# Kernel tuning notes

Measured on AMD Instinct MI355X. Metric: run time of the kernel, lower is better.

## Reference

```python
import jax, jax.numpy as jnp
import numpy as np
from jax import lax

AGG_HOPS = 3
RANK_K = 10
NEG = -1e9


def _aggregate(embs, agg_w, agg_b, W_last, b_last):
    # GIKT-style multi-hop mean aggregation: embs[j] has shape [B, n1..nj, D]
    embs = list(embs)
    for i in range(AGG_HOPS):
        for j in range(AGG_HOPS - i):
            s = jnp.mean(embs[j + 1], axis=-2) + embs[j]
            embs[j] = jnp.tanh(s @ agg_w[j].T + agg_b[j])
    return jnp.tanh(embs[0] @ W_last.T + b_last)


def _hops(nodes0, tabA, tabB):
    # alternating bipartite neighbor expansion: [B] -> [B,n] -> [B,n,n] -> ...
    lst = [nodes0]
    for i in range(AGG_HOPS):
        tab = tabA if i % 2 == 0 else tabB
        lst.append(tab[lst[-1]])
    return lst


def _forward(user, question, response, mask, q_neighbors, s_neighbors, u_neighbors,
             q_neighbors_2, qs_index, emb_question, emb_question_2, emb_skill,
             emb_user, emb_response, w1_q, w2_q, W_ih, W_hh, b_ih, b_hh,
             agg_w, agg_b, W_agg_last, b_agg_last, W_query, b_query, W_key, b_key,
             W_w, b_w, W_fusion, b_fusion):
    B, T = question.shape
    D = emb_question.shape[1]
    emb_q_all = emb_question[question]  # [B,T,D], used for recap similarity
    wA, wB = W_w[0, :D], W_w[0, D:]     # MLP_W(cat(Q,K)) = Q@wA + K@wB + b

    def predict(qs_concat, states, svalid):
        ql = (qs_concat @ W_query.T + b_query) @ wA          # [B,Lq]
        kl = (states @ W_key.T + b_key) @ wB                 # [B,Ls]
        logit = ql[:, :, None] + kl[:, None, :] + b_w[0]     # [B,Lq,Ls]
        logit = jnp.where(svalid[:, None, :], logit, NEG)
        Lq, Ls = logit.shape[1], logit.shape[2]
        alpha = jax.nn.softmax(logit.reshape(B, -1), axis=1).reshape(B, Lq, Ls)
        g = jnp.einsum('bqd,bsd->bqs', qs_concat, states)
        return jax.nn.sigmoid(jnp.sum(alpha * g, axis=(1, 2)))

    def step(carry, t):
        h, c, sh = carry
        q_t, u_t, r_t = question[:, t], user[:, t], response[:, t]
        m = (mask[:, t] == 1)[:, None]  # [B,1]
        # question-skill GNN branch
        embs_q = [(emb_question if i % 2 == 0 else emb_skill)[n]
                  for i, n in enumerate(_hops(q_t, q_neighbors, s_neighbors))]
        e1 = jnp.where(m, _aggregate(embs_q, agg_w, agg_b, W_agg_last, b_agg_last),
                       emb_question[q_t])
        # user-question GNN branch
        embs_u = [(emb_user if i % 2 == 0 else emb_question_2)[n]
                  for i, n in enumerate(_hops(u_t, u_neighbors, q_neighbors_2))]
        e2 = jnp.where(m, _aggregate(embs_u, agg_w, agg_b, W_agg_last, b_agg_last),
                       emb_question_2[q_t])
        e_hat = w1_q * e1 + w2_q * e2
        e_t = jax.nn.relu(jnp.concatenate([e_hat, emb_response[r_t]], axis=1)
                          @ W_fusion.T + b_fusion)
        # masked LSTMCell (torch gate order i,f,g,o); dropout in eval mode
        gates = e_t @ W_ih.T + b_ih + h @ W_hh.T + b_hh
        gi, gf, gg, go = jnp.split(gates, 4, axis=1)
        c2 = jax.nn.sigmoid(gf) * c + jax.nn.sigmoid(gi) * jnp.tanh(gg)
        h2 = jax.nn.sigmoid(go) * jnp.tanh(c2)
        h = jnp.where(m, h2, h)
        c = jnp.where(m, c2, c)
        sh = lax.dynamic_update_slice(sh, h[:, None, :], (0, t, 0))
        # next question + its related skills
        q_next = question[:, t + 1]
        emb_qn = emb_question[q_next]
        qs_concat = jnp.concatenate([emb_qn[:, None, :], emb_skill[qs_index[q_next]]], axis=1)
        # soft recap: top-k past states by (detached) question similarity
        scores = lax.stop_gradient(jnp.einsum('btd,bd->bt', emb_q_all, emb_qn))
        valid_t = jnp.arange(T) < t
        scores = jnp.where(valid_t[None, :], scores, NEG)
        _, idx = lax.top_k(scores, RANK_K)                    # [B,K]
        sel = jnp.take_along_axis(sh, idx[:, :, None], axis=1)  # [B,K,D]
        svalid = jnp.concatenate([jnp.ones((B, 1), bool), valid_t[idx]], axis=1)
        states = jnp.concatenate([h[:, None, :], sel], axis=1)  # [B,1+K,D]
        y = predict(qs_concat, states, svalid)
        return (h, c, sh), y

    h0 = jnp.zeros((B, D), jnp.float32)
    sh0 = jnp.zeros((B, T, D), jnp.float32)
    _, ys = lax.scan(step, (h0, h0, sh0), jnp.arange(T - 1))
    return jnp.concatenate([jnp.full((B, 1), 0.5, jnp.float32), ys.T], axis=1)


def setup_inputs() -> dict:
    B, T, D = 32, 50, 100
    NQ, NS, NU = 20000, 500, 10000
    NBR, SPQ = 6, 4
    key = jax.random.key(0)
    ks = iter(jax.random.split(key, 48))
    nrm = lambda shape, sc: jax.random.normal(next(ks), shape, jnp.float32) * sc
    ri = lambda shape, hi: jax.random.randint(next(ks), shape, 0, hi, jnp.int32)
    s = 1.0 / float(np.sqrt(D))
    return {
        'user': ri((B, T), NU), 'question': ri((B, T), NQ),
        'response': ri((B, T), 2), 'mask': ri((B, T), 2),
        'q_neighbors': ri((NQ, NBR), NS), 's_neighbors': ri((NS, NBR), NQ),
        'u_neighbors': ri((NU, NBR), NQ), 'q_neighbors_2': ri((NQ, NBR), NU),
        'qs_index': ri((NQ, SPQ), NS),
        'emb_question': nrm((NQ, D), 0.1), 'emb_question_2': nrm((NQ, D), 0.1),
        'emb_skill': nrm((NS, D), 0.1), 'emb_user': nrm((NU, D), 0.1),
        'emb_response': nrm((2, D), 0.1),
        'w1_q': jnp.float32(0.5), 'w2_q': jnp.float32(0.5),
        'W_ih': nrm((4 * D, D), s), 'W_hh': nrm((4 * D, D), s),
        'b_ih': jnp.zeros((4 * D,), jnp.float32), 'b_hh': jnp.zeros((4 * D,), jnp.float32),
        'agg_w': nrm((3, D, D), s), 'agg_b': jnp.zeros((3, D), jnp.float32),
        'W_agg_last': nrm((D, D), s), 'b_agg_last': jnp.zeros((D,), jnp.float32),
        'W_query': nrm((D, D), s), 'b_query': jnp.zeros((D,), jnp.float32),
        'W_key': nrm((D, D), s), 'b_key': jnp.zeros((D,), jnp.float32),
        'W_w': nrm((1, 2 * D), s), 'b_w': jnp.zeros((1,), jnp.float32),
        'W_fusion': nrm((D, 2 * D), s), 'b_fusion': jnp.zeros((D,), jnp.float32),
    }


def reference(user, question, response, mask, q_neighbors, s_neighbors, u_neighbors,
              q_neighbors_2, qs_index, emb_question, emb_question_2, emb_skill,
              emb_user, emb_response, w1_q, w2_q, W_ih, W_hh, b_ih, b_hh,
              agg_w, agg_b, W_agg_last, b_agg_last, W_query, b_query, W_key, b_key,
              W_w, b_w, W_fusion, b_fusion):
    return _forward(user, question, response, mask, q_neighbors, s_neighbors,
                    u_neighbors, q_neighbors_2, qs_index, emb_question,
                    emb_question_2, emb_skill, emb_user, emb_response, w1_q, w2_q,
                    W_ih, W_hh, b_ih, b_hh, agg_w, agg_b, W_agg_last, b_agg_last,
                    W_query, b_query, W_key, b_key, W_w, b_w, W_fusion, b_fusion)
```

## Files before the change

### kernel.cpp

```cpp
#include <hip/hip_runtime.h>
#include <hip/hip_bf16.h>

#define BSZ 32
#define TT 50
#define TS 49

#define OFF_VQ    0u
#define OFF_VK    128u
#define OFF_SC    256u
#define OFF_BIHH  288u
#define OFF_GPRE  704u
#define OFF_QL    627904u
#define OFF_IDX   640448u
#define OFF_NV    656128u
#define OFF_QSC   657696u
#define OFF_E1    1441696u
#define OFF_E2    1598496u

#define RLF(v,l) __uint_as_float(__builtin_amdgcn_readlane(__float_as_uint(v), (l)))

__device__ __forceinline__ float tanh_fast(float x) {
    float e = __expf(2.f * x);
    return 1.f - __fdividef(2.f, e + 1.f);
}
__device__ __forceinline__ float sigm_fast(float x) {
    return __fdividef(1.f, 1.f + __expf(-x));
}
__device__ __forceinline__ float dot4(float4 a, float4 b) {
    return a.x*b.x + a.y*b.y + a.z*b.z + a.w*b.w;
}
__device__ __forceinline__ float dot100(const float* __restrict__ w, const float* __restrict__ x) {
    float acc = 0.f;
    for (int k = 0; k < 100; k += 4)
        acc += dot4(*(const float4*)(w + k), *(const float4*)(x + k));
    return acc;
}

__global__ __launch_bounds__(256) void kprep(
    const float* __restrict__ wq, const float* __restrict__ bq,
    const float* __restrict__ wk, const float* __restrict__ bk,
    const float* __restrict__ ww, const float* __restrict__ bw,
    const float* __restrict__ w1, const float* __restrict__ w2,
    const float* __restrict__ bih, const float* __restrict__ bhh,
    float* __restrict__ WS)
{
    int tid = threadIdx.x;
    for (int i = tid; i < 400; i += 256) WS[OFF_BIHH + i] = bih[i] + bhh[i];
    if (tid < 100) {
        float a1 = 0.f, a2 = 0.f;
        for (int d = 0; d < 100; ++d) {
            a1 += ww[d]       * wq[d*100 + tid];
            a2 += ww[100 + d] * wk[d*100 + tid];
        }
        WS[OFF_VQ + tid] = a1;
        WS[OFF_VK + tid] = a2;
    }
    if (tid == 0) {
        float cq = 0.f, ck = 0.f;
        for (int d = 0; d < 100; ++d) {
            cq += bq[d] * ww[d];
            ck += bk[d] * ww[100 + d];
        }
        WS[OFF_SC + 0] = cq;
        WS[OFF_SC + 1] = ck;
        WS[OFF_SC + 2] = bw[0];
        WS[OFF_SC + 3] = w1[0];
        WS[OFF_SC + 4] = w2[0];
    }
}

__global__ __launch_bounds__(256) void kagg(
    const int* __restrict__ user, const int* __restrict__ question, const int* __restrict__ mask,
    const int* __restrict__ qnbr, const int* __restrict__ snbr,
    const int* __restrict__ unbr, const int* __restrict__ qnbr2,
    const float* __restrict__ embQ, const float* __restrict__ embQ2, const float* __restrict__ embS,
    const float* __restrict__ embU,
    const float* __restrict__ aggw, const float* __restrict__ aggb,
    const float* __restrict__ wlast, const float* __restrict__ blast,
    float* __restrict__ WS)
{
    int bid = blockIdx.x;
    int pair = bid >> 1, which = bid & 1;
    int b = pair / TS, t = pair - b*TS;
    int tid = threadIdx.x;
    int mm = mask[b*TT + t];
    float* outE = WS + (which ? OFF_E2 : OFF_E1) + (size_t)pair*100;

    if (mm != 1) {
        int q_t = question[b*TT + t];
        const float* src = which ? embQ2 : embQ;
        if (tid < 100) outE[tid] = src[(size_t)q_t*100 + tid];
        return;
    }

    int root = which ? user[b*TT + t] : question[b*TT + t];
    const int*   tabA = which ? unbr  : qnbr;
    const int*   tabB = which ? qnbr2 : snbr;
    const float* embE = which ? embU  : embQ;
    const float* embO = which ? embQ2 : embS;

    __shared__ __align__(16) float b2in[36*108];
    __shared__ __align__(16) float x1[6*108];
    __shared__ float s2[600], v1a[600], v1b[600];
    __shared__ __align__(16) float x0[104], v0a[104], v0b[104];
    __shared__ int n1[8], n2[36], n3[216];

    if (tid < 6) n1[tid] = tabA[root*6 + tid];
    __syncthreads();
    if (tid < 36) n2[tid] = tabB[n1[tid/6]*6 + (tid % 6)];
    __syncthreads();
    if (tid < 216) n3[tid] = tabA[n2[tid/6]*6 + (tid % 6)];
    __syncthreads();
    for (int e = tid; e < 3600; e += 256) {
        int v = e / 100, d = e - v*100;
        float acc = embE[(size_t)n2[v]*100 + d];
        float s3 = 0.f;
        const int* p = n3 + v*6;
        for (int c = 0; c < 6; ++c) s3 += embO[(size_t)p[c]*100 + d];
        b2in[v*108 + d] = acc + s3 * (1.f/6.f);
    }
    for (int e = tid; e < 600; e += 256) {
        int a = e / 100, d = e - a*100;
        float acc = embO[(size_t)n1[a]*100 + d];
        float s = 0.f;
        for (int c = 0; c < 6; ++c) s += embE[(size_t)n2[a*6 + c]*100 + d];
        x1[a*108 + d] = acc + s * (1.f/6.f);
    }
    if (tid < 100) {
        float acc = embE[(size_t)root*100 + tid];
        float s = 0.f;
        for (int a = 0; a < 6; ++a) s += embO[(size_t)n1[a]*100 + tid];
        x0[tid] = acc + s * (1.f/6.f);
    }
    __syncthreads();
    if (tid < 150) {
        int dblk = tid / 6, a = tid % 6, d0 = dblk*4;
        const float* wp = aggw + 20000 + d0*100;
        const float* xb = b2in + a*648;
        float acc[4][6];
        #pragma unroll
        for (int r = 0; r < 4; ++r)
            #pragma unroll
            for (int c = 0; c < 6; ++c) acc[r][c] = 0.f;
        #pragma unroll
        for (int j = 0; j < 25; ++j) {
            float4 r0 = *(const float4*)(wp + 4*j);
            float4 r1 = *(const float4*)(wp + 100 + 4*j);
            float4 r2 = *(const float4*)(wp + 200 + 4*j);
            float4 r3 = *(const float4*)(wp + 300 + 4*j);
            #pragma unroll
            for (int c = 0; c < 6; ++c) {
                float4 x = *(const float4*)(xb + c*108 + 4*j);
                acc[0][c] += dot4(r0, x);
                acc[1][c] += dot4(r1, x);
                acc[2][c] += dot4(r2, x);
                acc[3][c] += dot4(r3, x);
            }
        }
        #pragma unroll
        for (int r = 0; r < 4; ++r) {
            float bia = aggb[200 + d0 + r];
            float o = 0.f;
            #pragma unroll
            for (int c = 0; c < 6; ++c) o += tanh_fast(bia + acc[r][c]);
            s2[a*100 + d0 + r] = o;
        }
    } else if (tid < 200) {
        int d0 = (tid - 150)*2;
        const float* wp = aggw + 10000 + d0*100;
        float acc[2][6];
        #pragma unroll
        for (int r = 0; r < 2; ++r)
            #pragma unroll
            for (int c = 0; c < 6; ++c) acc[r][c] = 0.f;
        #pragma unroll
        for (int j = 0; j < 25; ++j) {
            float4 r0 = *(const float4*)(wp + 4*j);
            float4 r1 = *(const float4*)(wp + 100 + 4*j);
            #pragma unroll
            for (int c = 0; c < 6; ++c) {
                float4 x = *(const float4*)(x1 + c*108 + 4*j);
                acc[0][c] += dot4(r0, x);
                acc[1][c] += dot4(r1, x);
            }
        }
        #pragma unroll
        for (int r = 0; r < 2; ++r)
            #pragma unroll
            for (int c = 0; c < 6; ++c)
                v1a[c*100 + d0 + r] = tanh_fast(aggb[100 + d0 + r] + acc[r][c]);
    } else if (tid < 250) {
        int d0 = (tid - 200)*2;
        const float* wp = aggw + d0*100;
        float a0 = 0.f, a1 = 0.f;
        #pragma unroll
        for (int j = 0; j < 25; ++j) {
            float4 x  = *(const float4*)(x0 + 4*j);
            a0 += dot4(*(const float4*)(wp + 4*j), x);
            a1 += dot4(*(const float4*)(wp + 100 + 4*j), x);
        }
        v0a[d0]   = tanh_fast(aggb[d0] + a0);
        v0a[d0+1] = tanh_fast(aggb[d0+1] + a1);
    }
    __syncthreads();
    for (int e = tid; e < 600; e += 256) {
        int a = e / 100, d = e - a*100;
        x1[a*108 + d] = v1a[a*100 + d] + s2[a*100 + d]*(1.f/6.f);
    }
    if (tid < 100) {
        float s = 0.f;
        for (int a = 0; a < 6; ++a) s += v1a[a*100 + tid];
        x0[tid] = v0a[tid] + s*(1.f/6.f);
    }
    __syncthreads();
    if (tid < 50) {
        int d0 = tid*2;
        const float* wp = aggw + 10000 + d0*100;
        float acc[2][6];
        #pragma unroll
        for (int r = 0; r < 2; ++r)
            #pragma unroll
            for (int c = 0; c < 6; ++c) acc[r][c] = 0.f;
        #pragma unroll
        for (int j = 0; j < 25; ++j) {
            float4 r0 = *(const float4*)(wp + 4*j);
            float4 r1 = *(const float4*)(wp + 100 + 4*j);
            #pragma unroll
            for (int c = 0; c < 6; ++c) {
                float4 x = *(const float4*)(x1 + c*108 + 4*j);
                acc[0][c] += dot4(r0, x);
                acc[1][c] += dot4(r1, x);
            }
        }
        #pragma unroll
        for (int r = 0; r < 2; ++r)
            #pragma unroll
            for (int c = 0; c < 6; ++c)
                v1b[c*100 + d0 + r] = tanh_fast(aggb[100 + d0 + r] + acc[r][c]);
    } else if (tid >= 64 && tid < 114) {
        int d0 = (tid - 64)*2;
        const float* wp = aggw + d0*100;
        float a0 = 0.f, a1 = 0.f;
        #pragma unroll
        for (int j = 0; j < 25; ++j) {
            float4 x  = *(const float4*)(x0 + 4*j);
            a0 += dot4(*(const float4*)(wp + 4*j), x);
            a1 += dot4(*(const float4*)(wp + 100 + 4*j), x);
        }
        v0b[d0]   = tanh_fast(aggb[d0] + a0);
        v0b[d0+1] = tanh_fast(aggb[d0+1] + a1);
    }
    __syncthreads();
    if (tid < 100) {
        float s = 0.f;
        for (int a = 0; a < 6; ++a) s += v1b[a*100 + tid];
        x0[tid] = v0b[tid] + s*(1.f/6.f);
    }
    __syncthreads();
    if (tid < 50) {
        int d0 = tid*2;
        const float* wp = aggw + d0*100;
        float a0 = 0.f, a1 = 0.f;
        #pragma unroll
        for (int j = 0; j < 25; ++j) {
            float4 x  = *(const float4*)(x0 + 4*j);
            a0 += dot4(*(const float4*)(wp + 4*j), x);
            a1 += dot4(*(const float4*)(wp + 100 + 4*j), x);
        }
        v0a[d0]   = tanh_fast(aggb[d0] + a0);
        v0a[d0+1] = tanh_fast(aggb[d0+1] + a1);
    }
    __syncthreads();
    if (tid < 50) {
        int d0 = tid*2;
        const float* wp = wlast + d0*100;
        float a0 = 0.f, a1 = 0.f;
        #pragma unroll
        for (int j = 0; j < 25; ++j) {
            float4 x  = *(const float4*)(v0a + 4*j);
            a0 += dot4(*(const float4*)(wp + 4*j), x);
            a1 += dot4(*(const float4*)(wp + 100 + 4*j), x);
        }
        outE[d0]   = tanh_fast(blast[d0] + a0);
        outE[d0+1] = tanh_fast(blast[d0+1] + a1);
    }
}

__global__ __launch_bounds__(256) void kfuse(
    const int* __restrict__ question, const int* __restrict__ response,
    const int* __restrict__ qsidx,
    const float* __restrict__ embQ, const float* __restrict__ embS, const float* __restrict__ embR,
    const float* __restrict__ wfus, const float* __restrict__ bfus,
    const float* __restrict__ wih,
    float* __restrict__ WS)
{
    int bid = blockIdx.x;
    int b = bid / TS, t = bid - b*TS;
    int tid = threadIdx.x;
    size_t bt = (size_t)b*TS + t;

    __shared__ __align__(16) float sEIN[200], sET[104], sEQN[104];
    __shared__ float sQSCm[500], sScore[52];

    int r_t = response[b*TT + t];
    int qn  = question[b*TT + t + 1];
    float w1 = WS[OFF_SC + 3], w2s = WS[OFF_SC + 4];
    if (tid < 100)
        sEIN[tid] = w1*WS[OFF_E1 + bt*100 + tid] + w2s*WS[OFF_E2 + bt*100 + tid];
    else if (tid < 200)
        sEIN[tid] = embR[r_t*100 + (tid - 100)];
    __syncthreads();
    if (tid < 100) {
        float acc = bfus[tid];
        const float* wr = wfus + tid*200;
        for (int k = 0; k < 200; k += 4)
            acc += dot4(*(const float4*)(wr + k), *(const float4*)(sEIN + k));
        sET[tid] = fmaxf(acc, 0.f);
    } else if (tid >= 128 && tid < 228) {
        sEQN[tid - 128] = embQ[(size_t)qn*100 + (tid - 128)];
    }
    __syncthreads();
    for (int o = tid; o < 400; o += 256)
        WS[OFF_GPRE + bt*400 + o] = WS[OFF_BIHH + o] + dot100(wih + o*100, sET);
    for (int i = tid; i < 500; i += 256) {
        int q = i / 100, d = i - q*100;
        float val = (q == 0) ? sEQN[d] : embS[(size_t)qsidx[qn*4 + (q-1)]*100 + d];
        sQSCm[i] = val;
        WS[OFF_QSC + bt*500 + i] = val;
    }
    if (tid >= 200 && tid < 200 + TT) {
        int tp = tid - 200;
        if (tp < t) {
            int qq = question[b*TT + tp];
            float acc = 0.f;
            for (int k = 0; k < 100; ++k) acc += embQ[(size_t)qq*100 + k] * sEQN[k];
            sScore[tp] = acc;
        }
    }
    __syncthreads();
    if (tid < 5) {
        float acc = WS[OFF_SC + 0];
        for (int k = 0; k < 100; ++k) acc += sQSCm[tid*100 + k] * WS[OFF_VQ + k];
        WS[OFF_QL + bt*8 + tid] = acc;
    }
    if (tid == 64) {
        int nv = t < 10 ? t : 10;
        ((int*)(WS + OFF_NV))[bt] = nv;
        int* idxp = (int*)(WS + OFF_IDX) + bt*10;
        unsigned long long taken = 0ull;
        for (int p = 0; p < 10; ++p) {
            int bi = 0;
            if (p < nv) {
                float best = -3.0e38f;
                for (int tp2 = 0; tp2 < t; ++tp2) {
                    if (!((taken >> tp2) & 1ull) && sScore[tp2] > best) { best = sScore[tp2]; bi = tp2; }
                }
                taken |= (1ull << bi);
            }
            idxp[p] = bi;
        }
    }
}

__global__ __launch_bounds__(512) void kseq(
    const int* __restrict__ mask, const float* __restrict__ whh,
    const float* __restrict__ WS, float* __restrict__ out)
{
    int b = blockIdx.x, tid = threadIdx.x, lane = tid & 63;
    __shared__ float sQSCall[TS*500];
    __shared__ float sSH[TS*100];
    __shared__ float sQLall[TS*8];
    __shared__ int   sIdxAll[TS*10];
    __shared__ int   sNvAll[TS];
    __shared__ int   sMask[TT];
    __shared__ float sH[104], sC[104], sG[400], sVKl[104];
    __shared__ float sKL[12], sGv[64];

    const float* gGPRE = WS + OFF_GPRE;
    size_t b0 = (size_t)b*TS;

    float4 wv[25];
    if (tid < 400) {
        #pragma unroll
        for (int j = 0; j < 25; ++j) wv[j] = *(const float4*)(whh + tid*100 + 4*j);
    }
    float gpre = (tid < 400) ? gGPRE[b0*400 + tid] : 0.f;

    for (int i = tid; i < TS*500; i += 512) sQSCall[i] = WS[OFF_QSC + b0*500 + i];
    for (int i = tid; i < TS*8;   i += 512) sQLall[i]  = WS[OFF_QL + b0*8 + i];
    for (int i = tid; i < TS*10;  i += 512) sIdxAll[i] = ((const int*)(WS + OFF_IDX))[b0*10 + i];
    for (int i = tid; i < TS;     i += 512) sNvAll[i]  = ((const int*)(WS + OFF_NV))[b0 + i];
    if (tid < TT) sMask[tid] = mask[b*TT + tid];
    for (int i = tid; i < 104; i += 512) { sH[i] = 0.f; sC[i] = 0.f; sVKl[i] = (i < 100) ? WS[OFF_VK + i] : 0.f; }
    float ck = WS[OFF_SC + 1], bw = WS[OFF_SC + 2];
    if (tid == 0) out[b*TT] = 0.5f;
    __syncthreads();

    for (int t = 0; t < TS; ++t) {
        float gpre_nx = 0.f;
        if (tid < 400 && t + 1 < TS) gpre_nx = gGPRE[(b0 + t + 1)*400 + tid];

        float hA = sH[lane];
        float hB = sH[64 + (lane % 36)];
        if (tid < 400) {
            float a0 = 0.f, a1 = 0.f, a2 = 0.f, a3 = 0.f;
            #pragma unroll
            for (int j = 0; j < 25; ++j) {
                const int kb = 4*j;
                float h0, h1, h2, h3;
                if (kb < 64) {
                    h0 = RLF(hA, kb);   h1 = RLF(hA, kb+1);
                    h2 = RLF(hA, kb+2); h3 = RLF(hA, kb+3);
                } else {
                    h0 = RLF(hB, kb-64); h1 = RLF(hB, kb-63);
                    h2 = RLF(hB, kb-62); h3 = RLF(hB, kb-61);
                }
                a0 = fmaf(h0, wv[j].x, a0);
                a1 = fmaf(h1, wv[j].y, a1);
                a2 = fmaf(h2, wv[j].z, a2);
                a3 = fmaf(h3, wv[j].w, a3);
            }
            sG[tid] = (a0 + a1) + (a2 + a3) + gpre;
        }
        __syncthreads();
        if (tid < 100) {
            int mm = sMask[t];
            float gi = sG[tid], gf = sG[100+tid], gg = sG[200+tid], go = sG[300+tid];
            float c2 = sigm_fast(gf)*sC[tid] + sigm_fast(gi)*tanh_fast(gg);
            float h2 = sigm_fast(go)*tanh_fast(c2);
            if (mm == 1) { sH[tid] = h2; sC[tid] = c2; }
            sSH[t*100 + tid] = sH[tid];
        }
        __syncthreads();
        int nv = sNvAll[t];
        int k0 = tid & 15, slot = tid >> 4;
        const float* xq = sQSCall + t*500;
        #pragma unroll
        for (int p = 0; p < 3; ++p) {
            int id = p*32 + slot;
            float acc = 0.f;
            bool on = false, isKL = false; int q = 0, s = 0;
            if (id < 66) {
                isKL = id < 11;
                if (isKL) s = id; else { q = (id - 11) / 11; s = (id - 11) % 11; }
                if (s <= nv) {
                    on = true;
                    const float* st = (s == 0) ? sH : (sSH + sIdxAll[t*10 + s - 1]*100);
                    const float* xp = isKL ? sVKl : (xq + q*100);
                    #pragma unroll
                    for (int jj = 0; jj < 7; ++jj) {
                        int k = k0 + 16*jj;
                        if (k < 100) acc = fmaf(st[k], xp[k], acc);
                    }
                }
            }
            acc += __shfl_xor(acc, 1); acc += __shfl_xor(acc, 2);
            acc += __shfl_xor(acc, 4); acc += __shfl_xor(acc, 8);
            if (on && k0 == 0) { if (isKL) sKL[s] = acc + ck; else sGv[q*11 + s] = acc; }
        }
        __syncthreads();
        if (tid < 64) {
            int nst = nv + 1;
            int q = tid / 11, s = tid - q*11;
            bool valid = (tid < 55) && (s < nst);
            float lg = valid ? (sQLall[t*8 + q] + sKL[s] + bw) : -3.0e38f;
            float mx = lg;
            #pragma unroll
            for (int m = 1; m < 64; m <<= 1) mx = fmaxf(mx, __shfl_xor(mx, m));
            float e  = valid ? __expf(lg - mx) : 0.f;
            float gv = valid ? sGv[q*11 + s] : 0.f;
            float se = e, sg = e*gv;
            #pragma unroll
            for (int m = 1; m < 64; m <<= 1) { se += __shfl_xor(se, m); sg += __shfl_xor(sg, m); }
            if (tid == 0) out[b*TT + t + 1] = __fdividef(1.f, 1.f + __expf(-__fdividef(sg, se)));
        }
        gpre = gpre_nx;
        __syncthreads();
    }
}

extern "C" void kernel_launch(void* const* d_in, const int* in_sizes, int n_in,
                              void* d_out, int out_size, void* d_ws, size_t ws_size,
                              hipStream_t stream) {
    const int* user      = (const int*)d_in[0];
    const int* question  = (const int*)d_in[1];
    const int* response  = (const int*)d_in[2];
    const int* mask      = (const int*)d_in[3];
    const int* qnbr      = (const int*)d_in[4];
    const int* snbr      = (const int*)d_in[5];
    const int* unbr      = (const int*)d_in[6];
    const int* qnbr2     = (const int*)d_in[7];
    const int* qsidx     = (const int*)d_in[8];
    const float* embQ    = (const float*)d_in[9];
    const float* embQ2   = (const float*)d_in[10];
    const float* embS    = (const float*)d_in[11];
    const float* embU    = (const float*)d_in[12];
    const float* embR    = (const float*)d_in[13];
    const float* w1      = (const float*)d_in[14];
    const float* w2      = (const float*)d_in[15];
    const float* wih     = (const float*)d_in[16];
    const float* whh     = (const float*)d_in[17];
    const float* bih     = (const float*)d_in[18];
    const float* bhh     = (const float*)d_in[19];
    const float* aggw    = (const float*)d_in[20];
    const float* aggb    = (const float*)d_in[21];
    const float* wlast   = (const float*)d_in[22];
    const float* blast   = (const float*)d_in[23];
    const float* wq      = (const float*)d_in[24];
    const float* bq      = (const float*)d_in[25];
    const float* wk      = (const float*)d_in[26];
    const float* bk      = (const float*)d_in[27];
    const float* ww      = (const float*)d_in[28];
    const float* bwp     = (const float*)d_in[29];
    const float* wfus    = (const float*)d_in[30];
    const float* bfus    = (const float*)d_in[31];
    float* WS = (float*)d_ws;
    float* out = (float*)d_out;

    hipLaunchKernelGGL(kprep, dim3(1), dim3(256), 0, stream,
                       wq, bq, wk, bk, ww, bwp, w1, w2, bih, bhh, WS);
    hipLaunchKernelGGL(kagg, dim3(2*BSZ*TS), dim3(256), 0, stream,
                       user, question, mask, qnbr, snbr, unbr, qnbr2,
                       embQ, embQ2, embS, embU, aggw, aggb, wlast, blast, WS);
    hipLaunchKernelGGL(kfuse, dim3(BSZ*TS), dim3(256), 0, stream,
                       question, response, qsidx, embQ, embS, embR,
                       wfus, bfus, wih, WS);
    hipLaunchKernelGGL(kseq, dim3(BSZ), dim3(512), 0, stream,
                       mask, whh, WS, out);
}
```

Before: 489.2 us.

## Drop prep kernel, widen aggregation blocks, overlap attention with LSTM steps

Measured after the change: 438.4 us. 10.4% less time.

```diff
diff --git a/kernel.cpp b/kernel.cpp
--- a/kernel.cpp
+++ b/kernel.cpp
@@ -4,18 +4,15 @@
 #define BSZ 32
 #define TT 50
 #define TS 49
-
-#define OFF_VQ    0u
-#define OFF_VK    128u
-#define OFF_SC    256u
-#define OFF_BIHH  288u
-#define OFF_GPRE  704u
-#define OFF_QL    627904u
-#define OFF_IDX   640448u
-#define OFF_NV    656128u
-#define OFF_QSC   657696u
-#define OFF_E1    1441696u
-#define OFF_E2    1598496u
+#define PH 101
+
+#define OFF_GPRE  0u
+#define OFF_QL    627200u
+#define OFF_IDX   639744u
+#define OFF_NV    655424u
+#define OFF_QSC   656992u
+#define OFF_E1    1440992u
+#define OFF_E2    1597792u
 
 #define RLF(v,l) __uint_as_float(__builtin_amdgcn_readlane(__float_as_uint(v), (l)))
 
@@ -36,40 +33,7 @@
     return acc;
 }
 
-__global__ __launch_bounds__(256) void kprep(
-    const float* __restrict__ wq, const float* __restrict__ bq,
-    const float* __restrict__ wk, const float* __restrict__ bk,
-    const float* __restrict__ ww, const float* __restrict__ bw,
-    const float* __restrict__ w1, const float* __restrict__ w2,
-    const float* __restrict__ bih, const float* __restrict__ bhh,
-    float* __restrict__ WS)
-{
-    int tid = threadIdx.x;
-    for (int i = tid; i < 400; i += 256) WS[OFF_BIHH + i] = bih[i] + bhh[i];
-    if (tid < 100) {
-        float a1 = 0.f, a2 = 0.f;
-        for (int d = 0; d < 100; ++d) {
-            a1 += ww[d]       * wq[d*100 + tid];
-            a2 += ww[100 + d] * wk[d*100 + tid];
-        }
-        WS[OFF_VQ + tid] = a1;
-        WS[OFF_VK + tid] = a2;
-    }
-    if (tid == 0) {
-        float cq = 0.f, ck = 0.f;
-        for (int d = 0; d < 100; ++d) {
-            cq += bq[d] * ww[d];
-            ck += bk[d] * ww[100 + d];
-        }
-        WS[OFF_SC + 0] = cq;
-        WS[OFF_SC + 1] = ck;
-        WS[OFF_SC + 2] = bw[0];
-        WS[OFF_SC + 3] = w1[0];
-        WS[OFF_SC + 4] = w2[0];
-    }
-}
-
-__global__ __launch_bounds__(256) void kagg(
+__global__ __launch_bounds__(384, 5) void kagg(
     const int* __restrict__ user, const int* __restrict__ question, const int* __restrict__ mask,
     const int* __restrict__ qnbr, const int* __restrict__ snbr,
     const int* __restrict__ unbr, const int* __restrict__ qnbr2,
@@ -101,7 +65,8 @@
 
     __shared__ __align__(16) float b2in[36*108];
     __shared__ __align__(16) float x1[6*108];
-    __shared__ float s2[600], v1a[600], v1b[600];
+    __shared__ float s2v1b[600];
+    __shared__ float v1a[600];
     __shared__ __align__(16) float x0[104], v0a[104], v0b[104];
     __shared__ int n1[8], n2[36], n3[216];
 
@@ -111,7 +76,7 @@
     __syncthreads();
     if (tid < 216) n3[tid] = tabA[n2[tid/6]*6 + (tid % 6)];
     __syncthreads();
-    for (int e = tid; e < 3600; e += 256) {
+    for (int e = tid; e < 3600; e += 384) {
         int v = e / 100, d = e - v*100;
         float acc = embE[(size_t)n2[v]*100 + d];
         float s3 = 0.f;
@@ -119,7 +84,7 @@
         for (int c = 0; c < 6; ++c) s3 += embO[(size_t)p[c]*100 + d];
         b2in[v*108 + d] = acc + s3 * (1.f/6.f);
     }
-    for (int e = tid; e < 600; e += 256) {
+    for (int e = tid; e < 600; e += 384) {
         int a = e / 100, d = e - a*100;
         float acc = embO[(size_t)n1[a]*100 + d];
         float s = 0.f;
@@ -133,46 +98,35 @@
         x0[tid] = acc + s * (1.f/6.f);
     }
     __syncthreads();
-    if (tid < 150) {
-        int dblk = tid / 6, a = tid % 6, d0 = dblk*4;
+    if (tid < 300) {
+        int dblk = tid / 6, a = tid - dblk*6, d0 = dblk*2;
         const float* wp = aggw + 20000 + d0*100;
         const float* xb = b2in + a*648;
-        float acc[4][6];
-        #pragma unroll
-        for (int r = 0; r < 4; ++r)
-            #pragma unroll
-            for (int c = 0; c < 6; ++c) acc[r][c] = 0.f;
+        float a0[6], a1[6];
+        #pragma unroll
+        for (int c = 0; c < 6; ++c) { a0[c] = 0.f; a1[c] = 0.f; }
         #pragma unroll
         for (int j = 0; j < 25; ++j) {
             float4 r0 = *(const float4*)(wp + 4*j);
             float4 r1 = *(const float4*)(wp + 100 + 4*j);
-            float4 r2 = *(const float4*)(wp + 200 + 4*j);
-            float4 r3 = *(const float4*)(wp + 300 + 4*j);
             #pragma unroll
             for (int c = 0; c < 6; ++c) {
                 float4 x = *(const float4*)(xb + c*108 + 4*j);
-                acc[0][c] += dot4(r0, x);
-                acc[1][c] += dot4(r1, x);
-                acc[2][c] += dot4(r2, x);
-                acc[3][c] += dot4(r3, x);
-            }
-        }
-        #pragma unroll
-        for (int r = 0; r < 4; ++r) {
-            float bia = aggb[200 + d0 + r];
-            float o = 0.f;
-            #pragma unroll
-            for (int c = 0; c < 6; ++c) o += tanh_fast(bia + acc[r][c]);
-            s2[a*100 + d0 + r] = o;
-        }
-    } else if (tid < 200) {
-        int d0 = (tid - 150)*2;
+                a0[c] += dot4(r0, x);
+                a1[c] += dot4(r1, x);
+            }
+        }
+        float bi0 = aggb[200 + d0], bi1 = aggb[200 + d0 + 1];
+        float o0 = 0.f, o1 = 0.f;
+        #pragma unroll
+        for (int c = 0; c < 6; ++c) { o0 += tanh_fast(bi0 + a0[c]); o1 += tanh_fast(bi1 + a1[c]); }
+        s2v1b[a*100 + d0] = o0; s2v1b[a*100 + d0 + 1] = o1;
+    } else if (tid < 350) {
+        int d0 = (tid - 300)*2;
         const float* wp = aggw + 10000 + d0*100;
-        float acc[2][6];
-        #pragma unroll
-        for (int r = 0; r < 2; ++r)
-            #pragma unroll
-            for (int c = 0; c < 6; ++c) acc[r][c] = 0.f;
+        float a0[6], a1[6];
+        #pragma unroll
+        for (int c = 0; c < 6; ++c) { a0[c] = 0.f; a1[c] = 0.f; }
         #pragma unroll
         for (int j = 0; j < 25; ++j) {
             float4 r0 = *(const float4*)(wp + 4*j);
@@ -180,32 +134,36 @@
             #pragma unroll
             for (int c = 0; c < 6; ++c) {
                 float4 x = *(const float4*)(x1 + c*108 + 4*j);
-                acc[0][c] += dot4(r0, x);
-                acc[1][c] += dot4(r1, x);
-            }
-        }
-        #pragma unroll
-        for (int r = 0; r < 2; ++r)
-            #pragma unroll
-            for (int c = 0; c < 6; ++c)
-                v1a[c*100 + d0 + r] = tanh_fast(aggb[100 + d0 + r] + acc[r][c]);
-    } else if (tid < 250) {
-        int d0 = (tid - 200)*2;
+                a0[c] += dot4(r0, x);
+                a1[c] += dot4(r1, x);
+            }
+        }
+        #pragma unroll
+        for (int c = 0; c < 6; ++c) {
+            v1a[c*100 + d0]     = tanh_fast(aggb[100 + d0] + a0[c]);
+            v1a[c*100 + d0 + 1] = tanh_fast(aggb[100 + d0 + 1] + a1[c]);
+        }
+    } else if (tid < 375) {
+        int d0 = (tid - 350)*4;
         const float* wp = aggw + d0*100;
-        float a0 = 0.f, a1 = 0.f;
-        #pragma unroll
-        for (int j = 0; j < 25; ++j) {
-            float4 x  = *(const float4*)(x0 + 4*j);
+        float a0 = 0.f, a1 = 0.f, a2 = 0.f, a3 = 0.f;
+        #pragma unroll
+        for (int j = 0; j < 25; ++j) {
+            float4 x = *(const float4*)(x0 + 4*j);
             a0 += dot4(*(const float4*)(wp + 4*j), x);
             a1 += dot4(*(const float4*)(wp + 100 + 4*j), x);
+            a2 += dot4(*(const float4*)(wp + 200 + 4*j), x);
+            a3 += dot4(*(const float4*)(wp + 300 + 4*j), x);
         }
         v0a[d0]   = tanh_fast(aggb[d0] + a0);
         v0a[d0+1] = tanh_fast(aggb[d0+1] + a1);
-    }
-    __syncthreads();
-    for (int e = tid; e < 600; e += 256) {
+        v0a[d0+2] = tanh_fast(aggb[d0+2] + a2);
+        v0a[d0+3] = tanh_fast(aggb[d0+3] + a3);
+    }
+    __syncthreads();
+    for (int e = tid; e < 600; e += 384) {
         int a = e / 100, d = e - a*100;
-        x1[a*108 + d] = v1a[a*100 + d] + s2[a*100 + d]*(1.f/6.f);
+        x1[a*108 + d] = v1a[a*100 + d] + s2v1b[a*100 + d]*(1.f/6.f);
     }
     if (tid < 100) {
         float s = 0.f;
@@ -216,11 +174,9 @@
     if (tid < 50) {
         int d0 = tid*2;
         const float* wp = aggw + 10000 + d0*100;
-        float acc[2][6];
-        #pragma unroll
-        for (int r = 0; r < 2; ++r)
-            #pragma unroll
-            for (int c = 0; c < 6; ++c) acc[r][c] = 0.f;
+        float a0[6], a1[6];
+        #pragma unroll
+        for (int c = 0; c < 6; ++c) { a0[c] = 0.f; a1[c] = 0.f; }
         #pragma unroll
         for (int j = 0; j < 25; ++j) {
             float4 r0 = *(const float4*)(wp + 4*j);
@@ -228,61 +184,73 @@
             #pragma unroll
             for (int c = 0; c < 6; ++c) {
                 float4 x = *(const float4*)(x1 + c*108 + 4*j);
-                acc[0][c] += dot4(r0, x);
-                acc[1][c] += dot4(r1, x);
-            }
-        }
-        #pragma unroll
-        for (int r = 0; r < 2; ++r)
-            #pragma unroll
-            for (int c = 0; c < 6; ++c)
-                v1b[c*100 + d0 + r] = tanh_fast(aggb[100 + d0 + r] + acc[r][c]);
-    } else if (tid >= 64 && tid < 114) {
-        int d0 = (tid - 64)*2;
+                a0[c] += dot4(r0, x);
+                a1[c] += dot4(r1, x);
+            }
+        }
+        #pragma unroll
+        for (int c = 0; c < 6; ++c) {
+            s2v1b[c*100 + d0]     = tanh_fast(aggb[100 + d0] + a0[c]);
+            s2v1b[c*100 + d0 + 1] = tanh_fast(aggb[100 + d0 + 1] + a1[c]);
+        }
+    } else if (tid >= 64 && tid < 89) {
+        int d0 = (tid - 64)*4;
         const float* wp = aggw + d0*100;
-        float a0 = 0.f, a1 = 0.f;
-        #pragma unroll
-        for (int j = 0; j < 25; ++j) {
-            float4 x  = *(const float4*)(x0 + 4*j);
+        float a0 = 0.f, a1 = 0.f, a2 = 0.f, a3 = 0.f;
+        #pragma unroll
+        for (int j = 0; j < 25; ++j) {
+            float4 x = *(const float4*)(x0 + 4*j);
             a0 += dot4(*(const float4*)(wp + 4*j), x);
             a1 += dot4(*(const float4*)(wp + 100 + 4*j), x);
+            a2 += dot4(*(const float4*)(wp + 200 + 4*j), x);
+            a3 += dot4(*(const float4*)(wp + 300 + 4*j), x);
         }
         v0b[d0]   = tanh_fast(aggb[d0] + a0);
         v0b[d0+1] = tanh_fast(aggb[d0+1] + a1);
+        v0b[d0+2] = tanh_fast(aggb[d0+2] + a2);
+        v0b[d0+3] = tanh_fast(aggb[d0+3] + a3);
     }
     __syncthreads();
     if (tid < 100) {
         float s = 0.f;
-        for (int a = 0; a < 6; ++a) s += v1b[a*100 + tid];
+        for (int a = 0; a < 6; ++a) s += s2v1b[a*100 + tid];
         x0[tid] = v0b[tid] + s*(1.f/6.f);
     }
     __syncthreads();
-    if (tid < 50) {
-        int d0 = tid*2;
+    if (tid < 25) {
+        int d0 = tid*4;
         const float* wp = aggw + d0*100;
-        float a0 = 0.f, a1 = 0.f;
-        #pragma unroll
-        for (int j = 0; j < 25; ++j) {
-            float4 x  = *(const float4*)(x0 + 4*j);
+        float a0 = 0.f, a1 = 0.f, a2 = 0.f, a3 = 0.f;
+        #pragma unroll
+        for (int j = 0; j < 25; ++j) {
+            float4 x = *(const float4*)(x0 + 4*j);
             a0 += dot4(*(const float4*)(wp + 4*j), x);
             a1 += dot4(*(const float4*)(wp + 100 + 4*j), x);
+            a2 += dot4(*(const float4*)(wp + 200 + 4*j), x);
+            a3 += dot4(*(const float4*)(wp + 300 + 4*j), x);
         }
         v0a[d0]   = tanh_fast(aggb[d0] + a0);
         v0a[d0+1] = tanh_fast(aggb[d0+1] + a1);
-    }
-    __syncthreads();
-    if (tid < 50) {
-        int d0 = tid*2;
+        v0a[d0+2] = tanh_fast(aggb[d0+2] + a2);
+        v0a[d0+3] = tanh_fast(aggb[d0+3] + a3);
+    }
+    __syncthreads();
+    if (tid < 25) {
+        int d0 = tid*4;
         const float* wp = wlast + d0*100;
-        float a0 = 0.f, a1 = 0.f;
-        #pragma unroll
-        for (int j = 0; j < 25; ++j) {
-            float4 x  = *(const float4*)(v0a + 4*j);
+        float a0 = 0.f, a1 = 0.f, a2 = 0.f, a3 = 0.f;
+        #pragma unroll
+        for (int j = 0; j < 25; ++j) {
+            float4 x = *(const float4*)(v0a + 4*j);
             a0 += dot4(*(const float4*)(wp + 4*j), x);
             a1 += dot4(*(const float4*)(wp + 100 + 4*j), x);
+            a2 += dot4(*(const float4*)(wp + 200 + 4*j), x);
+            a3 += dot4(*(const float4*)(wp + 300 + 4*j), x);
         }
         outE[d0]   = tanh_fast(blast[d0] + a0);
         outE[d0+1] = tanh_fast(blast[d0+1] + a1);
+        outE[d0+2] = tanh_fast(blast[d0+2] + a2);
+        outE[d0+3] = tanh_fast(blast[d0+3] + a3);
     }
 }
 
@@ -290,8 +258,10 @@
     const int* __restrict__ question, const int* __restrict__ response,
     const int* __restrict__ qsidx,
     const float* __restrict__ embQ, const float* __restrict__ embS, const float* __restrict__ embR,
+    const float* __restrict__ w1p, const float* __restrict__ w2p,
     const float* __restrict__ wfus, const float* __restrict__ bfus,
-    const float* __restrict__ wih,
+    const float* __restrict__ wih, const float* __restrict__ bih, const float* __restrict__ bhh,
+    const float* __restrict__ wq, const float* __restrict__ bq, const float* __restrict__ ww,
     float* __restrict__ WS)
 {
     int bid = blockIdx.x;
@@ -299,16 +269,18 @@
     int tid = threadIdx.x;
     size_t bt = (size_t)b*TS + t;
 
-    __shared__ __align__(16) float sEIN[200], sET[104], sEQN[104];
-    __shared__ float sQSCm[500], sScore[52];
+    __shared__ __align__(16) float sEIN[200], sET[104], sEQN[104], sVQ[104];
+    __shared__ float sWW[200], sQSCm[500], sScore[56], sCq[1];
 
     int r_t = response[b*TT + t];
     int qn  = question[b*TT + t + 1];
-    float w1 = WS[OFF_SC + 3], w2s = WS[OFF_SC + 4];
+    float w1 = w1p[0], w2 = w2p[0];
     if (tid < 100)
-        sEIN[tid] = w1*WS[OFF_E1 + bt*100 + tid] + w2s*WS[OFF_E2 + bt*100 + tid];
+        sEIN[tid] = w1*WS[OFF_E1 + bt*100 + tid] + w2*WS[OFF_E2 + bt*100 + tid];
     else if (tid < 200)
         sEIN[tid] = embR[r_t*100 + (tid - 100)];
+    else
+        for (int i = tid - 200; i < 200; i += 56) sWW[i] = ww[i];
     __syncthreads();
     if (tid < 100) {
         float acc = bfus[tid];
@@ -316,34 +288,55 @@
         for (int k = 0; k < 200; k += 4)
             acc += dot4(*(const float4*)(wr + k), *(const float4*)(sEIN + k));
         sET[tid] = fmaxf(acc, 0.f);
-    } else if (tid >= 128 && tid < 228) {
-        sEQN[tid - 128] = embQ[(size_t)qn*100 + (tid - 128)];
-    }
-    __syncthreads();
-    for (int o = tid; o < 400; o += 256)
-        WS[OFF_GPRE + bt*400 + o] = WS[OFF_BIHH + o] + dot100(wih + o*100, sET);
-    for (int i = tid; i < 500; i += 256) {
-        int q = i / 100, d = i - q*100;
-        float val = (q == 0) ? sEQN[d] : embS[(size_t)qsidx[qn*4 + (q-1)]*100 + d];
-        sQSCm[i] = val;
-        WS[OFF_QSC + bt*500 + i] = val;
-    }
-    if (tid >= 200 && tid < 200 + TT) {
+    } else if (tid < 200) {
+        int k = tid - 100;
+        float acc = 0.f;
+        for (int d = 0; d < 100; ++d) acc += sWW[d]*wq[d*100 + k];
+        sVQ[k] = acc;
+    } else if (tid == 200) {
+        float acc = 0.f;
+        for (int d = 0; d < 100; ++d) acc += bq[d]*sWW[d];
+        sCq[0] = acc;
+    } else if (tid >= 201 && tid < 251) {
+        int d = tid - 201;
+        sEQN[d]      = embQ[(size_t)qn*100 + d];
+        sEQN[d + 50] = embQ[(size_t)qn*100 + d + 50];
+    }
+    __syncthreads();
+    if (tid < 200) {
+        for (int i = tid; i < 500; i += 200) {
+            int q = i / 100, d = i - q*100;
+            float val = (q == 0) ? sEQN[d] : embS[(size_t)qsidx[qn*4 + (q-1)]*100 + d];
+            sQSCm[i] = val;
+            WS[OFF_QSC + bt*500 + i] = val;
+        }
+    } else if (tid < 250) {
         int tp = tid - 200;
         if (tp < t) {
             int qq = question[b*TT + tp];
+            const float* er = embQ + (size_t)qq*100;
             float acc = 0.f;
-            for (int k = 0; k < 100; ++k) acc += embQ[(size_t)qq*100 + k] * sEQN[k];
+            for (int k = 0; k < 100; k += 4)
+                acc += dot4(*(const float4*)(er + k), *(const float4*)(sEQN + k));
             sScore[tp] = acc;
         }
     }
     __syncthreads();
-    if (tid < 5) {
-        float acc = WS[OFF_SC + 0];
-        for (int k = 0; k < 100; ++k) acc += sQSCm[tid*100 + k] * WS[OFF_VQ + k];
-        WS[OFF_QL + bt*8 + tid] = acc;
-    }
-    if (tid == 64) {
+    for (int o = tid; o < 400; o += 256)
+        WS[OFF_GPRE + bt*400 + o] = bih[o] + bhh[o] + dot100(wih + o*100, sET);
+    if (tid < 80) {
+        int q = tid >> 4, k0 = tid & 15;
+        float acc = 0.f;
+        #pragma unroll
+        for (int j = 0; j < 7; ++j) {
+            int k = k0 + 16*j;
+            if (k < 100) acc = fmaf(sQSCm[q*100 + k], sVQ[k], acc);
+        }
+        acc += __shfl_xor(acc, 1); acc += __shfl_xor(acc, 2);
+        acc += __shfl_xor(acc, 4); acc += __shfl_xor(acc, 8);
+        if (k0 == 0) WS[OFF_QL + bt*8 + q] = acc + sCq[0];
+    }
+    if (tid == 255) {
         int nv = t < 10 ? t : 10;
         ((int*)(WS + OFF_NV))[bt] = nv;
         int* idxp = (int*)(WS + OFF_IDX) + bt*10;
@@ -362,47 +355,62 @@
     }
 }
 
-__global__ __launch_bounds__(512) void kseq(
+__global__ __launch_bounds__(576) void kseq(
     const int* __restrict__ mask, const float* __restrict__ whh,
+    const float* __restrict__ wk, const float* __restrict__ bk,
+    const float* __restrict__ ww, const float* __restrict__ bwp,
     const float* __restrict__ WS, float* __restrict__ out)
 {
     int b = blockIdx.x, tid = threadIdx.x, lane = tid & 63;
     __shared__ float sQSCall[TS*500];
-    __shared__ float sSH[TS*100];
+    __shared__ float sSH[TS*PH + 3];
     __shared__ float sQLall[TS*8];
     __shared__ int   sIdxAll[TS*10];
     __shared__ int   sNvAll[TS];
     __shared__ int   sMask[TT];
     __shared__ float sH[104], sC[104], sG[400], sVKl[104];
-    __shared__ float sKL[12], sGv[64];
-
-    const float* gGPRE = WS + OFF_GPRE;
+    __shared__ float sKL2[2][12], sGv2[2][64];
+    __shared__ float sCkBw[2];
+
     size_t b0 = (size_t)b*TS;
+    int g = tid - 64;
+    bool isGate = (g >= 0 && g < 400);
 
     float4 wv[25];
-    if (tid < 400) {
-        #pragma unroll
-        for (int j = 0; j < 25; ++j) wv[j] = *(const float4*)(whh + tid*100 + 4*j);
-    }
-    float gpre = (tid < 400) ? gGPRE[b0*400 + tid] : 0.f;
-
-    for (int i = tid; i < TS*500; i += 512) sQSCall[i] = WS[OFF_QSC + b0*500 + i];
-    for (int i = tid; i < TS*8;   i += 512) sQLall[i]  = WS[OFF_QL + b0*8 + i];
-    for (int i = tid; i < TS*10;  i += 512) sIdxAll[i] = ((const int*)(WS + OFF_IDX))[b0*10 + i];
-    for (int i = tid; i < TS;     i += 512) sNvAll[i]  = ((const int*)(WS + OFF_NV))[b0 + i];
+    if (isGate) {
+        #pragma unroll
+        for (int j = 0; j < 25; ++j) wv[j] = *(const float4*)(whh + g*100 + 4*j);
+    }
+    float gpre = isGate ? WS[OFF_GPRE + b0*400 + g] : 0.f;
+
+    for (int i = tid; i < TS*500; i += 576) sQSCall[i] = WS[OFF_QSC + b0*500 + i];
+    for (int i = tid; i < TS*8;   i += 576) sQLall[i]  = WS[OFF_QL + b0*8 + i];
+    for (int i = tid; i < TS*10;  i += 576) sIdxAll[i] = ((const int*)(WS + OFF_IDX))[b0*10 + i];
+    for (int i = tid; i < TS;     i += 576) sNvAll[i]  = ((const int*)(WS + OFF_NV))[b0 + i];
     if (tid < TT) sMask[tid] = mask[b*TT + tid];
-    for (int i = tid; i < 104; i += 512) { sH[i] = 0.f; sC[i] = 0.f; sVKl[i] = (i < 100) ? WS[OFF_VK + i] : 0.f; }
-    float ck = WS[OFF_SC + 1], bw = WS[OFF_SC + 2];
-    if (tid == 0) out[b*TT] = 0.5f;
-    __syncthreads();
+    if (tid < 104) { sH[tid] = 0.f; sC[tid] = 0.f; }
+    if (tid >= 104 && tid < 204) {
+        int k = tid - 104;
+        float acc = 0.f;
+        for (int d = 0; d < 100; ++d) acc += ww[100 + d]*wk[d*100 + k];
+        sVKl[k] = acc;
+    }
+    if (tid == 204) {
+        float acc = 0.f;
+        for (int d = 0; d < 100; ++d) acc += bk[d]*ww[100 + d];
+        sCkBw[0] = acc; sCkBw[1] = bwp[0];
+    }
+    if (tid == 205) out[b*TT] = 0.5f;
+    __syncthreads();
+    float ck = sCkBw[0], bw = sCkBw[1];
 
     for (int t = 0; t < TS; ++t) {
-        float gpre_nx = 0.f;
-        if (tid < 400 && t + 1 < TS) gpre_nx = gGPRE[(b0 + t + 1)*400 + tid];
-
-        float hA = sH[lane];
-        float hB = sH[64 + (lane % 36)];
-        if (tid < 400) {
+        int par = t & 1;
+        if (isGate) {
+            float hA = sH[lane];
+            float hB = sH[64 + (lane % 36)];
+            float gpre_nx = 0.f;
+            if (t + 1 < TS) gpre_nx = WS[OFF_GPRE + (b0 + t + 1)*400 + g];
             float a0 = 0.f, a1 = 0.f, a2 = 0.f, a3 = 0.f;
             #pragma unroll
             for (int j = 0; j < 25; ++j) {
@@ -420,62 +428,95 @@
                 a2 = fmaf(h2, wv[j].z, a2);
                 a3 = fmaf(h3, wv[j].w, a3);
             }
-            sG[tid] = (a0 + a1) + (a2 + a3) + gpre;
-        }
-        __syncthreads();
-        if (tid < 100) {
-            int mm = sMask[t];
-            float gi = sG[tid], gf = sG[100+tid], gg = sG[200+tid], go = sG[300+tid];
-            float c2 = sigm_fast(gf)*sC[tid] + sigm_fast(gi)*tanh_fast(gg);
-            float h2 = sigm_fast(go)*tanh_fast(c2);
-            if (mm == 1) { sH[tid] = h2; sC[tid] = c2; }
-            sSH[t*100 + tid] = sH[tid];
-        }
-        __syncthreads();
-        int nv = sNvAll[t];
-        int k0 = tid & 15, slot = tid >> 4;
-        const float* xq = sQSCall + t*500;
-        #pragma unroll
-        for (int p = 0; p < 3; ++p) {
-            int id = p*32 + slot;
-            float acc = 0.f;
-            bool on = false, isKL = false; int q = 0, s = 0;
-            if (id < 66) {
-                isKL = id < 11;
-                if (isKL) s = id; else { q = (id - 11) / 11; s = (id - 11) % 11; }
+            sG[g] = (a0 + a1) + (a2 + a3) + gpre;
+            gpre = gpre_nx;
+        } else if (tid >= 512) {
+            int nv = sNvAll[t];
+            if (lane < 60) {
+                bool isKL = lane < 10;
+                int s = isKL ? (lane + 1) : (((lane - 10) % 10) + 1);
+                int q = isKL ? 0 : ((lane - 10) / 10);
                 if (s <= nv) {
-                    on = true;
-                    const float* st = (s == 0) ? sH : (sSH + sIdxAll[t*10 + s - 1]*100);
-                    const float* xp = isKL ? sVKl : (xq + q*100);
+                    const float* st = sSH + sIdxAll[t*10 + s - 1]*PH;
+                    const float* xp = isKL ? sVKl : (sQSCall + t*500 + q*100);
+                    float c0 = 0.f, c1 = 0.f, c2 = 0.f, c3 = 0.f;
                     #pragma unroll
-                    for (int jj = 0; jj < 7; ++jj) {
-                        int k = k0 + 16*jj;
-                        if (k < 100) acc = fmaf(st[k], xp[k], acc);
+                    for (int k = 0; k < 100; k += 4) {
+                        c0 = fmaf(st[k],   xp[k],   c0);
+                        c1 = fmaf(st[k+1], xp[k+1], c1);
+                        c2 = fmaf(st[k+2], xp[k+2], c2);
+                        c3 = fmaf(st[k+3], xp[k+3], c3);
                     }
+                    float acc = (c0 + c1) + (c2 + c3);
+                    if (isKL) sKL2[par][s] = acc + ck;
+                    else      sGv2[par][q*12 + s] = acc;
                 }
             }
-            acc += __shfl_xor(acc, 1); acc += __shfl_xor(acc, 2);
-            acc += __shfl_xor(acc, 4); acc += __shfl_xor(acc, 8);
-            if (on && k0 == 0) { if (isKL) sKL[s] = acc + ck; else sGv[q*11 + s] = acc; }
-        }
-        __syncthreads();
-        if (tid < 64) {
-            int nst = nv + 1;
-            int q = tid / 11, s = tid - q*11;
-            bool valid = (tid < 55) && (s < nst);
-            float lg = valid ? (sQLall[t*8 + q] + sKL[s] + bw) : -3.0e38f;
-            float mx = lg;
-            #pragma unroll
-            for (int m = 1; m < 64; m <<= 1) mx = fmaxf(mx, __shfl_xor(mx, m));
-            float e  = valid ? __expf(lg - mx) : 0.f;
-            float gv = valid ? sGv[q*11 + s] : 0.f;
+        } else if (tid < 64 && t > 0) {
+            int tau = t - 1, par2 = tau & 1;
+            int nv = sNvAll[tau];
+            int dd = lane >> 3, k0 = lane & 7;
+            if (dd < 6) {
+                const float* xp = (dd == 0) ? sVKl : (sQSCall + tau*500 + (dd-1)*100);
+                float acc = 0.f;
+                #pragma unroll
+                for (int jj = 0; jj < 13; ++jj) {
+                    int k = k0 + 8*jj;
+                    if (k < 100) acc = fmaf(sH[k], xp[k], acc);
+                }
+                acc += __shfl_xor(acc, 1); acc += __shfl_xor(acc, 2); acc += __shfl_xor(acc, 4);
+                if (k0 == 0) {
+                    if (dd == 0) sKL2[par2][0] = acc + ck;
+                    else         sGv2[par2][(dd-1)*12] = acc;
+                }
+            }
+            int q = lane / 11, s = lane - q*11;
+            bool valid = (lane < 55) && (s <= nv);
+            float lg = valid ? (sQLall[tau*8 + q] + sKL2[par2][s] + bw) : 0.f;
+            float e  = valid ? __expf(lg) : 0.f;
+            float gv = valid ? sGv2[par2][q*12 + s] : 0.f;
             float se = e, sg = e*gv;
             #pragma unroll
             for (int m = 1; m < 64; m <<= 1) { se += __shfl_xor(se, m); sg += __shfl_xor(sg, m); }
-            if (tid == 0) out[b*TT + t + 1] = __fdividef(1.f, 1.f + __expf(-__fdividef(sg, se)));
-        }
-        gpre = gpre_nx;
+            if (lane == 0) out[b*TT + tau + 1] = __fdividef(1.f, 1.f + __expf(-__fdividef(sg, se)));
+        }
         __syncthreads();
+        if (g >= 0 && g < 100) {
+            float gi = sG[g], gf = sG[100+g], gg = sG[200+g], go = sG[300+g];
+            float c2 = sigm_fast(gf)*sC[g] + sigm_fast(gi)*tanh_fast(gg);
+            float h2 = sigm_fast(go)*tanh_fast(c2);
+            if (sMask[t] == 1) { sH[g] = h2; sC[g] = c2; }
+            sSH[t*PH + g] = sH[g];
+        }
+        __syncthreads();
+    }
+    if (tid < 64) {
+        int tau = TS - 1, par2 = tau & 1;
+        int nv = sNvAll[tau];
+        int dd = lane >> 3, k0 = lane & 7;
+        if (dd < 6) {
+            const float* xp = (dd == 0) ? sVKl : (sQSCall + tau*500 + (dd-1)*100);
+            float acc = 0.f;
+            #pragma unroll
+            for (int jj = 0; jj < 13; ++jj) {
+                int k = k0 + 8*jj;
+                if (k < 100) acc = fmaf(sH[k], xp[k], acc);
+            }
+            acc += __shfl_xor(acc, 1); acc += __shfl_xor(acc, 2); acc += __shfl_xor(acc, 4);
+            if (k0 == 0) {
+                if (dd == 0) sKL2[par2][0] = acc + ck;
+                else         sGv2[par2][(dd-1)*12] = acc;
+            }
+        }
+        int q = lane / 11, s = lane - q*11;
+        bool valid = (lane < 55) && (s <= nv);
+        float lg = valid ? (sQLall[tau*8 + q] + sKL2[par2][s] + bw) : 0.f;
+        float e  = valid ? __expf(lg) : 0.f;
+        float gv = valid ? sGv2[par2][q*12 + s] : 0.f;
+        float se = e, sg = e*gv;
+        #pragma unroll
+        for (int m = 1; m < 64; m <<= 1) { se += __shfl_xor(se, m); sg += __shfl_xor(sg, m); }
+        if (lane == 0) out[b*TT + tau + 1] = __fdividef(1.f, 1.f + __expf(-__fdividef(sg, se)));
     }
 }
 
@@ -517,14 +558,12 @@
     float* WS = (float*)d_ws;
     float* out = (float*)d_out;
 
-    hipLaunchKernelGGL(kprep, dim3(1), dim3(256), 0, stream,
-                       wq, bq, wk, bk, ww, bwp, w1, w2, bih, bhh, WS);
-    hipLaunchKernelGGL(kagg, dim3(2*BSZ*TS), dim3(256), 0, stream,
+    hipLaunchKernelGGL(kagg, dim3(2*BSZ*TS), dim3(384), 0, stream,
                        user, question, mask, qnbr, snbr, unbr, qnbr2,
                        embQ, embQ2, embS, embU, aggw, aggb, wlast, blast, WS);
     hipLaunchKernelGGL(kfuse, dim3(BSZ*TS), dim3(256), 0, stream,
                        question, response, qsidx, embQ, embS, embR,
-                       wfus, bfus, wih, WS);
-    hipLaunchKernelGGL(kseq, dim3(BSZ), dim3(512), 0, stream,
-                       mask, whh, WS, out);
-}
+                       w1, w2, wfus, bfus, wih, bih, bhh, wq, bq, ww, WS);
+    hipLaunchKernelGGL(kseq, dim3(BSZ), dim3(576), 0, stream,
+                       mask, whh, wk, bk, ww, bwp, WS, out);
+}
```
